# Optimization experiments

Hardware: AMD Instinct MI355X
Metric: run time of the kernel (lower is better)

The kernel has to match this reference:

```python
import jax, jax.numpy as jnp
import numpy as np

NEG_INF = -9e15
ALPHA = 0.2  # LeakyReLU negative slope

N = 4096
NFEAT = 512
NHID = 256
NEMBED = 128
NHEADS = 4
OUT1 = NHID // NHEADS   # 64
OUT2 = NEMBED // NHEADS # 32


def _gat_layer(x, adj_mask, W, a):
    # x: [N, F_in]; adj_mask: [N, N] bool; W: [H, F_in, F_out]; a: [H, 2*F_out]
    Fo = W.shape[-1]
    Wh = jnp.einsum('nf,hfo->hno', x, W)                     # [H, N, Fo]
    a_src = jnp.einsum('hno,ho->hn', Wh, a[:, :Fo])          # [H, N]
    a_dst = jnp.einsum('hno,ho->hn', Wh, a[:, Fo:])          # [H, N]
    e = a_src[:, :, None] + a_dst[:, None, :]                # [H, N, N]
    e = jax.nn.leaky_relu(e, negative_slope=ALPHA)
    e = jnp.where(adj_mask[None, :, :], e, NEG_INF)
    att = jax.nn.softmax(e, axis=-1)                         # [H, N, N]
    h = jnp.einsum('hnm,hmo->hno', att, Wh)                  # [H, N, Fo]
    h = jax.nn.elu(h)                                        # concat=True -> ELU
    # concat heads: [N, H*Fo]
    return jnp.transpose(h, (1, 0, 2)).reshape(x.shape[0], -1)


def setup_inputs() -> dict:
    key = jax.random.key(0)
    k1, k2, k3, k4, k5, k6 = jax.random.split(key, 6)
    x = jax.random.normal(k1, (N, NFEAT), dtype=jnp.float32)
    adj = (jax.random.uniform(k2, (N, N)) < 0.01).astype(jnp.float32)
    # per-head GAT params, xavier-uniform-like init (stacked over heads)
    def xavier(k, shape, fan):
        bound = np.sqrt(6.0 / fan)
        return jax.random.uniform(k, shape, minval=-bound, maxval=bound, dtype=jnp.float32)
    W1 = xavier(k3, (NHEADS, NFEAT, OUT1), NFEAT + OUT1)
    a1 = xavier(k4, (NHEADS, 2 * OUT1), 2 * OUT1 + 1)
    W2 = xavier(k5, (NHEADS, NHID, OUT2), NHID + OUT2)
    a2 = xavier(k6, (NHEADS, 2 * OUT2), 2 * OUT2 + 1)
    return {'x': x, 'adj': adj, 'W1': W1, 'a1': a1, 'W2': W2, 'a2': a2}


def reference(x, adj, W1, a1, W2, a2):
    # eval mode: dropout is identity
    adj_mask = adj > 0
    h1 = _gat_layer(x, adj_mask, W1, a1)    # [N, NHID]
    h2 = _gat_layer(h1, adj_mask, W2, a2)   # [N, NEMBED]
    return h2
```

## Files before the change

kernel.cpp:

```cpp
#include <hip/hip_runtime.h>
#include <hip/hip_bf16.h>
#include <cstdint>
#include <cstddef>

#define NNODES 4096
#define NHEADS 4
#define NBR_STRIDE 128

typedef __attribute__((ext_vector_type(8))) short bf16x8v;
typedef __attribute__((ext_vector_type(4))) float f32x4;

__device__ inline unsigned short bf16_rn(float f) {
    unsigned int u = __float_as_uint(f);
    u += 0x7FFFu + ((u >> 16) & 1u);
    return (unsigned short)(u >> 16);
}
__device__ inline float bf16_f32(unsigned short s) {
    return __uint_as_float(((unsigned int)s) << 16);
}

__global__ __launch_bounds__(256) void build_nbr_kernel(
    const float* __restrict__ adj, int* __restrict__ nbr, int* __restrict__ deg) {
    int wave = threadIdx.x >> 6;
    int lane = threadIdx.x & 63;
    int row = blockIdx.x * 4 + wave;
    const float4* arow = reinterpret_cast<const float4*>(adj + (size_t)row * NNODES);
    unsigned long long lt = (1ull << lane) - 1ull;
    int base = 0;
    #pragma unroll 4
    for (int it = 0; it < NNODES / 256; ++it) {
        float4 v = arow[it * 64 + lane];
        bool b0 = v.x > 0.f, b1 = v.y > 0.f, b2 = v.z > 0.f, b3 = v.w > 0.f;
        unsigned long long m0 = __ballot(b0);
        unsigned long long m1 = __ballot(b1);
        unsigned long long m2 = __ballot(b2);
        unsigned long long m3 = __ballot(b3);
        int pre = __popcll(m0 & lt) + __popcll(m1 & lt) +
                  __popcll(m2 & lt) + __popcll(m3 & lt);
        int pos = base + pre;
        int colb = it * 256 + lane * 4;
        if (b0) { if (pos < NBR_STRIDE) nbr[row * NBR_STRIDE + pos] = colb;     pos++; }
        if (b1) { if (pos < NBR_STRIDE) nbr[row * NBR_STRIDE + pos] = colb + 1; pos++; }
        if (b2) { if (pos < NBR_STRIDE) nbr[row * NBR_STRIDE + pos] = colb + 2; pos++; }
        if (b3) { if (pos < NBR_STRIDE) nbr[row * NBR_STRIDE + pos] = colb + 3; pos++; }
        base += __popcll(m0) + __popcll(m1) + __popcll(m2) + __popcll(m3);
    }
    if (lane == 0) deg[row] = base < NBR_STRIDE ? base : NBR_STRIDE;
}

__global__ __launch_bounds__(256) void pack_b_both_kernel(
    const float* __restrict__ W1, const float* __restrict__ W2,
    unsigned short* __restrict__ B1h, unsigned short* __restrict__ B1l,
    unsigned short* __restrict__ B2h, unsigned short* __restrict__ B2l) {
    int t = blockIdx.x * 256 + threadIdx.x;
    if (t < 256 * 512) {
        int n = t >> 9, k = t & 511;
        int h = n >> 6, o = n & 63;
        float v = W1[((size_t)h * 512 + k) * 64 + o];
        unsigned short hi = bf16_rn(v);
        B1h[t] = hi;
        B1l[t] = bf16_rn(v - bf16_f32(hi));
    } else {
        int u = t - 256 * 512;
        if (u < 128 * 256) {
            int n = u >> 8, k = u & 255;
            int h = n >> 5, o = n & 31;
            float v = W2[((size_t)h * 256 + k) * 32 + o];
            unsigned short hi = bf16_rn(v);
            B2h[u] = hi;
            B2l[u] = bf16_rn(v - bf16_f32(hi));
        }
    }
}

template <int K, int N>
__global__ __launch_bounds__(256) void gemm_split_kernel(
    const float* __restrict__ A,
    const unsigned short* __restrict__ Bh, const unsigned short* __restrict__ Bl,
    float* __restrict__ C) {
    constexpr int BM = 32, BN = 64, BK = 64, LP = BK + 8;
    __shared__ unsigned short Alh[BM][LP], All[BM][LP];
    __shared__ unsigned short Blh[BN][LP], Bll[BN][LP];
    int tid = threadIdx.x;
    int wave = tid >> 6, lane = tid & 63;
    int rowBase = blockIdx.x * BM;
    int colBase = blockIdx.y * BN;
    int wr = wave >> 1, wc = wave & 1;
    int lr = lane & 15, lk = lane >> 4;
    f32x4 acc0 = {0.f, 0.f, 0.f, 0.f};
    f32x4 acc1 = {0.f, 0.f, 0.f, 0.f};
    int ar = tid >> 3;
    int ac = (tid & 7) * 8;
    for (int k0 = 0; k0 < K; k0 += BK) {
        float4 a0 = *reinterpret_cast<const float4*>(&A[(size_t)(rowBase + ar) * K + k0 + ac]);
        float4 a1 = *reinterpret_cast<const float4*>(&A[(size_t)(rowBase + ar) * K + k0 + ac + 4]);
        uint4 bh0 = *reinterpret_cast<const uint4*>(&Bh[(size_t)(colBase + ar) * K + k0 + ac]);
        uint4 bl0 = *reinterpret_cast<const uint4*>(&Bl[(size_t)(colBase + ar) * K + k0 + ac]);
        uint4 bh1 = *reinterpret_cast<const uint4*>(&Bh[(size_t)(colBase + 32 + ar) * K + k0 + ac]);
        uint4 bl1 = *reinterpret_cast<const uint4*>(&Bl[(size_t)(colBase + 32 + ar) * K + k0 + ac]);
        __syncthreads();
        ushort4 h4, l4;
        h4.x = bf16_rn(a0.x); l4.x = bf16_rn(a0.x - bf16_f32(h4.x));
        h4.y = bf16_rn(a0.y); l4.y = bf16_rn(a0.y - bf16_f32(h4.y));
        h4.z = bf16_rn(a0.z); l4.z = bf16_rn(a0.z - bf16_f32(h4.z));
        h4.w = bf16_rn(a0.w); l4.w = bf16_rn(a0.w - bf16_f32(h4.w));
        *reinterpret_cast<ushort4*>(&Alh[ar][ac]) = h4;
        *reinterpret_cast<ushort4*>(&All[ar][ac]) = l4;
        h4.x = bf16_rn(a1.x); l4.x = bf16_rn(a1.x - bf16_f32(h4.x));
        h4.y = bf16_rn(a1.y); l4.y = bf16_rn(a1.y - bf16_f32(h4.y));
        h4.z = bf16_rn(a1.z); l4.z = bf16_rn(a1.z - bf16_f32(h4.z));
        h4.w = bf16_rn(a1.w); l4.w = bf16_rn(a1.w - bf16_f32(h4.w));
        *reinterpret_cast<ushort4*>(&Alh[ar][ac + 4]) = h4;
        *reinterpret_cast<ushort4*>(&All[ar][ac + 4]) = l4;
        *reinterpret_cast<uint4*>(&Blh[ar][ac]) = bh0;
        *reinterpret_cast<uint4*>(&Bll[ar][ac]) = bl0;
        *reinterpret_cast<uint4*>(&Blh[32 + ar][ac]) = bh1;
        *reinterpret_cast<uint4*>(&Bll[32 + ar][ac]) = bl1;
        __syncthreads();
        #pragma unroll
        for (int ks = 0; ks < 2; ++ks) {
            int kb = ks * 32 + lk * 8;
            bf16x8v ah = *reinterpret_cast<const bf16x8v*>(&Alh[wr * 16 + lr][kb]);
            bf16x8v al = *reinterpret_cast<const bf16x8v*>(&All[wr * 16 + lr][kb]);
            bf16x8v b0h = *reinterpret_cast<const bf16x8v*>(&Blh[wc * 32 + lr][kb]);
            bf16x8v b0l = *reinterpret_cast<const bf16x8v*>(&Bll[wc * 32 + lr][kb]);
            bf16x8v b1h = *reinterpret_cast<const bf16x8v*>(&Blh[wc * 32 + 16 + lr][kb]);
            bf16x8v b1l = *reinterpret_cast<const bf16x8v*>(&Bll[wc * 32 + 16 + lr][kb]);
            acc0 = __builtin_amdgcn_mfma_f32_16x16x32_bf16(ah, b0h, acc0, 0, 0, 0);
            acc0 = __builtin_amdgcn_mfma_f32_16x16x32_bf16(ah, b0l, acc0, 0, 0, 0);
            acc0 = __builtin_amdgcn_mfma_f32_16x16x32_bf16(al, b0h, acc0, 0, 0, 0);
            acc1 = __builtin_amdgcn_mfma_f32_16x16x32_bf16(ah, b1h, acc1, 0, 0, 0);
            acc1 = __builtin_amdgcn_mfma_f32_16x16x32_bf16(ah, b1l, acc1, 0, 0, 0);
            acc1 = __builtin_amdgcn_mfma_f32_16x16x32_bf16(al, b1h, acc1, 0, 0, 0);
        }
    }
    int crow = rowBase + wr * 16 + lk * 4;
    int ccol = colBase + wc * 32 + lr;
    #pragma unroll
    for (int r = 0; r < 4; ++r) {
        C[(size_t)(crow + r) * N + ccol]      = acc0[r];
        C[(size_t)(crow + r) * N + ccol + 16] = acc1[r];
    }
}

template <int FO>
__global__ __launch_bounds__(256) void adot_kernel(
    const float* __restrict__ Wh, const float* __restrict__ a,
    float* __restrict__ asrc, float* __restrict__ adst) {
    int t = blockIdx.x * blockDim.x + threadIdx.x;
    if (t >= NNODES * NHEADS) return;
    int n = t >> 2, h = t & 3;
    const float4* row = reinterpret_cast<const float4*>(Wh + (size_t)n * (NHEADS * FO) + h * FO);
    const float4* ah  = reinterpret_cast<const float4*>(a + h * 2 * FO);
    float s = 0.f, d = 0.f;
    #pragma unroll
    for (int o = 0; o < FO / 4; ++o) {
        float4 w = row[o];
        float4 u = ah[o];
        float4 v = ah[o + FO / 4];
        s += w.x * u.x + w.y * u.y + w.z * u.z + w.w * u.w;
        d += w.x * v.x + w.y * v.y + w.z * v.z + w.w * v.w;
    }
    asrc[h * NNODES + n] = s;
    adst[h * NNODES + n] = d;
}

template <int FO>
__global__ __launch_bounds__(256) void agg_kernel(
    const float* __restrict__ Wh,
    const float* __restrict__ asrc, const float* __restrict__ adst,
    const int* __restrict__ nbr, const int* __restrict__ deg,
    float* __restrict__ out) {
    __shared__ float2 sw[4][NBR_STRIDE];
    int wslot = threadIdx.x >> 6;
    int lane = threadIdx.x & 63;
    int wid = blockIdx.x * 4 + wslot;
    int n = wid >> 2, h = wid & 3;
    int dg = deg[n];
    const int* lst = nbr + n * NBR_STRIDE;
    float my_as = asrc[h * NNODES + n];

    int c0 = 0, c1 = 0;
    float e0 = -1e30f, e1 = -1e30f;
    if (lane < dg) {
        c0 = lst[lane];
        float e = my_as + adst[h * NNODES + c0];
        e0 = e >= 0.f ? e : 0.2f * e;
    }
    if (lane + 64 < dg) {
        c1 = lst[lane + 64];
        float e = my_as + adst[h * NNODES + c1];
        e1 = e >= 0.f ? e : 0.2f * e;
    }
    float m = fmaxf(e0, e1);
    #pragma unroll
    for (int s = 32; s; s >>= 1) m = fmaxf(m, __shfl_xor(m, s));
    float p0 = (lane < dg) ? __expf(e0 - m) : 0.f;
    float p1 = (lane + 64 < dg) ? __expf(e1 - m) : 0.f;
    float denom = p0 + p1;
    #pragma unroll
    for (int s = 32; s; s >>= 1) denom += __shfl_xor(denom, s);
    float inv = 1.0f / denom;

    if (lane < dg)      sw[wslot][lane]      = make_float2(p0 * inv, __int_as_float(c0));
    if (lane + 64 < dg) sw[wslot][lane + 64] = make_float2(p1 * inv, __int_as_float(c1));
    __syncthreads();

    constexpr int STRIDE = NHEADS * FO;
    constexpr int LPR = FO / 4;
    constexpr int NPS = 64 / LPR;
    int sub = lane / LPR;
    int dim4 = (lane % LPR) * 4;
    const float* whp = Wh + h * FO + dim4;
    f32x4 acc = {0.f, 0.f, 0.f, 0.f};
    int main_n = (dg / (4 * NPS)) * (4 * NPS);
    int k = 0;
    for (; k < main_n; k += 4 * NPS) {
        #pragma unroll
        for (int u = 0; u < 4; ++u) {
            float2 w = sw[wslot][k + u * NPS + sub];
            int col = __float_as_int(w.y);
            float4 v = *reinterpret_cast<const float4*>(&whp[(size_t)col * STRIDE]);
            acc[0] += w.x * v.x;
            acc[1] += w.x * v.y;
            acc[2] += w.x * v.z;
            acc[3] += w.x * v.w;
        }
    }
    for (; k < dg; k += NPS) {
        if (k + sub < dg) {
            float2 w = sw[wslot][k + sub];
            int col = __float_as_int(w.y);
            float4 v = *reinterpret_cast<const float4*>(&whp[(size_t)col * STRIDE]);
            acc[0] += w.x * v.x;
            acc[1] += w.x * v.y;
            acc[2] += w.x * v.z;
            acc[3] += w.x * v.w;
        }
    }
    #pragma unroll
    for (int s = LPR; s < 64; s <<= 1) {
        acc[0] += __shfl_xor(acc[0], s);
        acc[1] += __shfl_xor(acc[1], s);
        acc[2] += __shfl_xor(acc[2], s);
        acc[3] += __shfl_xor(acc[3], s);
    }
    if (lane < LPR) {
        float4 r;
        r.x = acc[0] > 0.f ? acc[0] : expm1f(acc[0]);
        r.y = acc[1] > 0.f ? acc[1] : expm1f(acc[1]);
        r.z = acc[2] > 0.f ? acc[2] : expm1f(acc[2]);
        r.w = acc[3] > 0.f ? acc[3] : expm1f(acc[3]);
        *reinterpret_cast<float4*>(&out[(size_t)n * STRIDE + h * FO + dim4]) = r;
    }
}

extern "C" void kernel_launch(void* const* d_in, const int* in_sizes, int n_in,
                              void* d_out, int out_size, void* d_ws, size_t ws_size,
                              hipStream_t stream) {
    const float* x   = (const float*)d_in[0];
    const float* adj = (const float*)d_in[1];
    const float* W1  = (const float*)d_in[2];
    const float* a1  = (const float*)d_in[3];
    const float* W2  = (const float*)d_in[4];
    const float* a2  = (const float*)d_in[5];
    float* out = (float*)d_out;

    char* p = (char*)d_ws;
    auto alloc = [&](size_t bytes) -> void* {
        void* r = (void*)p;
        p += (bytes + 255) & ~(size_t)255;
        return r;
    };
    int*   nbr = (int*)alloc((size_t)NNODES * NBR_STRIDE * 4);
    int*   deg = (int*)alloc((size_t)NNODES * 4);
    unsigned short* B1h = (unsigned short*)alloc((size_t)256 * 512 * 2);
    unsigned short* B1l = (unsigned short*)alloc((size_t)256 * 512 * 2);
    unsigned short* B2h = (unsigned short*)alloc((size_t)128 * 256 * 2);
    unsigned short* B2l = (unsigned short*)alloc((size_t)128 * 256 * 2);
    float* Wh1 = (float*)alloc((size_t)NNODES * 256 * 4);
    float* as1 = (float*)alloc((size_t)NHEADS * NNODES * 4);
    float* ad1 = (float*)alloc((size_t)NHEADS * NNODES * 4);
    float* h1  = (float*)alloc((size_t)NNODES * 256 * 4);
    float* Wh2 = (float*)alloc((size_t)NNODES * 128 * 4);
    float* as2 = (float*)alloc((size_t)NHEADS * NNODES * 4);
    float* ad2 = (float*)alloc((size_t)NHEADS * NNODES * 4);

    pack_b_both_kernel<<<dim3((256 * 512 + 128 * 256) / 256), dim3(256), 0, stream>>>(
        W1, W2, B1h, B1l, B2h, B2l);
    build_nbr_kernel<<<dim3(NNODES / 4), dim3(256), 0, stream>>>(adj, nbr, deg);

    gemm_split_kernel<512, 256><<<dim3(NNODES / 32, 256 / 64), dim3(256), 0, stream>>>(
        x, B1h, B1l, Wh1);
    adot_kernel<64><<<dim3(NNODES * NHEADS / 256), dim3(256), 0, stream>>>(
        Wh1, a1, as1, ad1);
    agg_kernel<64><<<dim3(NNODES * NHEADS / 4), dim3(256), 0, stream>>>(
        Wh1, as1, ad1, nbr, deg, h1);

    gemm_split_kernel<256, 128><<<dim3(NNODES / 32, 128 / 64), dim3(256), 0, stream>>>(
        h1, B2h, B2l, Wh2);
    adot_kernel<32><<<dim3(NNODES * NHEADS / 256), dim3(256), 0, stream>>>(
        Wh2, a2, as2, ad2);
    agg_kernel<32><<<dim3(NNODES * NHEADS / 4), dim3(256), 0, stream>>>(
        Wh2, as2, ad2, nbr, deg, out);
}
```

Measured before the change: 77.90 us.

## Fuse weight packing, attention dot products and neighbor build into GEMM kernels

Removes the separate weight pre-pack kernel: each GEMM block now loads fp32 W directly and splits it into bf16 hi/lo in shared memory. The a_src/a_dst dot products are computed in the GEMM epilogue with cross-lane shuffles and a small shared-memory reduction, which drops the adot kernels. Neighbor-list construction runs in the same launch as the first GEMM by partitioning blocks. Together this cuts the launch count from 8 to 4 and avoids re-reading Wh, at the cost of redundant weight conversion in every block and transposed, likely bank-conflicting LDS stores for B.

```diff
diff --git a/kernel.cpp b/kernel.cpp
--- a/kernel.cpp
+++ b/kernel.cpp
@@ -19,11 +19,12 @@
     return __uint_as_float(((unsigned int)s) << 16);
 }
 
-__global__ __launch_bounds__(256) void build_nbr_kernel(
-    const float* __restrict__ adj, int* __restrict__ nbr, int* __restrict__ deg) {
+__device__ inline void build_nbr_body(
+    const float* __restrict__ adj, int* __restrict__ nbr, int* __restrict__ deg,
+    int rowblk) {
     int wave = threadIdx.x >> 6;
     int lane = threadIdx.x & 63;
-    int row = blockIdx.x * 4 + wave;
+    int row = rowblk * 4 + wave;
     const float4* arow = reinterpret_cast<const float4*>(adj + (size_t)row * NNODES);
     unsigned long long lt = (1ull << lane) - 1ull;
     int base = 0;
@@ -48,43 +49,20 @@
     if (lane == 0) deg[row] = base < NBR_STRIDE ? base : NBR_STRIDE;
 }
 
-__global__ __launch_bounds__(256) void pack_b_both_kernel(
-    const float* __restrict__ W1, const float* __restrict__ W2,
-    unsigned short* __restrict__ B1h, unsigned short* __restrict__ B1l,
-    unsigned short* __restrict__ B2h, unsigned short* __restrict__ B2l) {
-    int t = blockIdx.x * 256 + threadIdx.x;
-    if (t < 256 * 512) {
-        int n = t >> 9, k = t & 511;
-        int h = n >> 6, o = n & 63;
-        float v = W1[((size_t)h * 512 + k) * 64 + o];
-        unsigned short hi = bf16_rn(v);
-        B1h[t] = hi;
-        B1l[t] = bf16_rn(v - bf16_f32(hi));
-    } else {
-        int u = t - 256 * 512;
-        if (u < 128 * 256) {
-            int n = u >> 8, k = u & 255;
-            int h = n >> 5, o = n & 31;
-            float v = W2[((size_t)h * 256 + k) * 32 + o];
-            unsigned short hi = bf16_rn(v);
-            B2h[u] = hi;
-            B2l[u] = bf16_rn(v - bf16_f32(hi));
-        }
-    }
-}
-
-template <int K, int N>
-__global__ __launch_bounds__(256) void gemm_split_kernel(
-    const float* __restrict__ A,
-    const unsigned short* __restrict__ Bh, const unsigned short* __restrict__ Bl,
-    float* __restrict__ C) {
+template <int K, int N, int FO>
+__device__ inline void gemm_body(
+    const float* __restrict__ A, const float* __restrict__ W,
+    const float* __restrict__ a, float* __restrict__ C,
+    float* __restrict__ asrc, float* __restrict__ adst,
+    int bx, int by) {
     constexpr int BM = 32, BN = 64, BK = 64, LP = BK + 8;
     __shared__ unsigned short Alh[BM][LP], All[BM][LP];
     __shared__ unsigned short Blh[BN][LP], Bll[BN][LP];
+    __shared__ float reds[2][BM], redd[2][BM];
     int tid = threadIdx.x;
     int wave = tid >> 6, lane = tid & 63;
-    int rowBase = blockIdx.x * BM;
-    int colBase = blockIdx.y * BN;
+    int rowBase = bx * BM;
+    int colBase = by * BN;
     int wr = wave >> 1, wc = wave & 1;
     int lr = lane & 15, lk = lane >> 4;
     f32x4 acc0 = {0.f, 0.f, 0.f, 0.f};
@@ -94,10 +72,19 @@
     for (int k0 = 0; k0 < K; k0 += BK) {
         float4 a0 = *reinterpret_cast<const float4*>(&A[(size_t)(rowBase + ar) * K + k0 + ac]);
         float4 a1 = *reinterpret_cast<const float4*>(&A[(size_t)(rowBase + ar) * K + k0 + ac + 4]);
-        uint4 bh0 = *reinterpret_cast<const uint4*>(&Bh[(size_t)(colBase + ar) * K + k0 + ac]);
-        uint4 bl0 = *reinterpret_cast<const uint4*>(&Bl[(size_t)(colBase + ar) * K + k0 + ac]);
-        uint4 bh1 = *reinterpret_cast<const uint4*>(&Bh[(size_t)(colBase + 32 + ar) * K + k0 + ac]);
-        uint4 bl1 = *reinterpret_cast<const uint4*>(&Bl[(size_t)(colBase + 32 + ar) * K + k0 + ac]);
+        float4 bw[4];
+        int bkr[4], bc4[4], bo[4], bh[4];
+        #pragma unroll
+        for (int i = 0; i < 4; ++i) {
+            int idx = tid + i * 256;
+            bkr[i] = idx >> 4;
+            bc4[i] = (idx & 15) * 4;
+            int n0 = colBase + bc4[i];
+            bh[i] = n0 / FO;
+            bo[i] = n0 % FO;
+            bw[i] = *reinterpret_cast<const float4*>(
+                &W[((size_t)bh[i] * K + k0 + bkr[i]) * FO + bo[i]]);
+        }
         __syncthreads();
         ushort4 h4, l4;
         h4.x = bf16_rn(a0.x); l4.x = bf16_rn(a0.x - bf16_f32(h4.x));
@@ -112,10 +99,19 @@
         h4.w = bf16_rn(a1.w); l4.w = bf16_rn(a1.w - bf16_f32(h4.w));
         *reinterpret_cast<ushort4*>(&Alh[ar][ac + 4]) = h4;
         *reinterpret_cast<ushort4*>(&All[ar][ac + 4]) = l4;
-        *reinterpret_cast<uint4*>(&Blh[ar][ac]) = bh0;
-        *reinterpret_cast<uint4*>(&Bll[ar][ac]) = bl0;
-        *reinterpret_cast<uint4*>(&Blh[32 + ar][ac]) = bh1;
-        *reinterpret_cast<uint4*>(&Bll[32 + ar][ac]) = bl1;
+        #pragma unroll
+        for (int i = 0; i < 4; ++i) {
+            float4 v = bw[i];
+            unsigned short hh, ll;
+            hh = bf16_rn(v.x); ll = bf16_rn(v.x - bf16_f32(hh));
+            Blh[bc4[i] + 0][bkr[i]] = hh; Bll[bc4[i] + 0][bkr[i]] = ll;
+            hh = bf16_rn(v.y); ll = bf16_rn(v.y - bf16_f32(hh));
+            Blh[bc4[i] + 1][bkr[i]] = hh; Bll[bc4[i] + 1][bkr[i]] = ll;
+            hh = bf16_rn(v.z); ll = bf16_rn(v.z - bf16_f32(hh));
+            Blh[bc4[i] + 2][bkr[i]] = hh; Bll[bc4[i] + 2][bkr[i]] = ll;
+            hh = bf16_rn(v.w); ll = bf16_rn(v.w - bf16_f32(hh));
+            Blh[bc4[i] + 3][bkr[i]] = hh; Bll[bc4[i] + 3][bkr[i]] = ll;
+        }
         __syncthreads();
         #pragma unroll
         for (int ks = 0; ks < 2; ++ks) {
@@ -141,28 +137,68 @@
         C[(size_t)(crow + r) * N + ccol]      = acc0[r];
         C[(size_t)(crow + r) * N + ccol + 16] = acc1[r];
     }
-}
-
-template <int FO>
-__global__ __launch_bounds__(256) void adot_kernel(
-    const float* __restrict__ Wh, const float* __restrict__ a,
-    float* __restrict__ asrc, float* __restrict__ adst) {
-    int t = blockIdx.x * blockDim.x + threadIdx.x;
-    if (t >= NNODES * NHEADS) return;
-    int n = t >> 2, h = t & 3;
-    const float4* row = reinterpret_cast<const float4*>(Wh + (size_t)n * (NHEADS * FO) + h * FO);
-    const float4* ah  = reinterpret_cast<const float4*>(a + h * 2 * FO);
-    float s = 0.f, d = 0.f;
-    #pragma unroll
-    for (int o = 0; o < FO / 4; ++o) {
-        float4 w = row[o];
-        float4 u = ah[o];
-        float4 v = ah[o + FO / 4];
-        s += w.x * u.x + w.y * u.y + w.z * u.z + w.w * u.w;
-        d += w.x * v.x + w.y * v.y + w.z * v.z + w.w * v.w;
-    }
-    asrc[h * NNODES + n] = s;
-    adst[h * NNODES + n] = d;
+    int n0 = colBase + wc * 32 + lr;
+    int hh = n0 / FO;
+    int o0 = n0 % FO;
+    int o1 = o0 + 16;
+    const float* av = a + hh * 2 * FO;
+    float aS0 = av[o0], aS1 = av[o1];
+    float aD0 = av[FO + o0], aD1 = av[FO + o1];
+    float sv[4], dv[4];
+    #pragma unroll
+    for (int r = 0; r < 4; ++r) {
+        sv[r] = acc0[r] * aS0 + acc1[r] * aS1;
+        dv[r] = acc0[r] * aD0 + acc1[r] * aD1;
+        #pragma unroll
+        for (int msk = 1; msk < 16; msk <<= 1) {
+            sv[r] += __shfl_xor(sv[r], msk);
+            dv[r] += __shfl_xor(dv[r], msk);
+        }
+    }
+    if constexpr (FO == 64) {
+        if (lr == 0) {
+            #pragma unroll
+            for (int r = 0; r < 4; ++r) {
+                reds[wc][wr * 16 + lk * 4 + r] = sv[r];
+                redd[wc][wr * 16 + lk * 4 + r] = dv[r];
+            }
+        }
+        __syncthreads();
+        if (tid < BM) {
+            int row = tid;
+            asrc[by * NNODES + rowBase + row] = reds[0][row] + reds[1][row];
+            adst[by * NNODES + rowBase + row] = redd[0][row] + redd[1][row];
+        }
+    } else {
+        if (lr == 0) {
+            #pragma unroll
+            for (int r = 0; r < 4; ++r) {
+                asrc[hh * NNODES + rowBase + wr * 16 + lk * 4 + r] = sv[r];
+                adst[hh * NNODES + rowBase + wr * 16 + lk * 4 + r] = dv[r];
+            }
+        }
+    }
+}
+
+__global__ __launch_bounds__(256) void fused1_kernel(
+    const float* __restrict__ adj, int* __restrict__ nbr, int* __restrict__ deg,
+    const float* __restrict__ x, const float* __restrict__ W1,
+    const float* __restrict__ a1, float* __restrict__ Wh1,
+    float* __restrict__ as1, float* __restrict__ ad1) {
+    int b = blockIdx.x;
+    if (b < NNODES / 4) {
+        build_nbr_body(adj, nbr, deg, b);
+    } else {
+        int g = b - NNODES / 4;
+        gemm_body<512, 256, 64>(x, W1, a1, Wh1, as1, ad1, g & 127, g >> 7);
+    }
+}
+
+__global__ __launch_bounds__(256) void gemm2_kernel(
+    const float* __restrict__ h1, const float* __restrict__ W2,
+    const float* __restrict__ a2, float* __restrict__ Wh2,
+    float* __restrict__ as2, float* __restrict__ ad2) {
+    gemm_body<256, 128, 32>(h1, W2, a2, Wh2, as2, ad2, blockIdx.x, blockIdx.y);
 }
 
 template <int FO>
@@ -274,10 +310,6 @@
     };
     int*   nbr = (int*)alloc((size_t)NNODES * NBR_STRIDE * 4);
     int*   deg = (int*)alloc((size_t)NNODES * 4);
-    unsigned short* B1h = (unsigned short*)alloc((size_t)256 * 512 * 2);
-    unsigned short* B1l = (unsigned short*)alloc((size_t)256 * 512 * 2);
-    unsigned short* B2h = (unsigned short*)alloc((size_t)128 * 256 * 2);
-    unsigned short* B2l = (unsigned short*)alloc((size_t)128 * 256 * 2);
     float* Wh1 = (float*)alloc((size_t)NNODES * 256 * 4);
     float* as1 = (float*)alloc((size_t)NHEADS * NNODES * 4);
     float* ad1 = (float*)alloc((size_t)NHEADS * NNODES * 4);
@@ -286,21 +318,13 @@
     float* as2 = (float*)alloc((size_t)NHEADS * NNODES * 4);
     float* ad2 = (float*)alloc((size_t)NHEADS * NNODES * 4);
 
-    pack_b_both_kernel<<<dim3((256 * 512 + 128 * 256) / 256), dim3(256), 0, stream>>>(
-        W1, W2, B1h, B1l, B2h, B2l);
-    build_nbr_kernel<<<dim3(NNODES / 4), dim3(256), 0, stream>>>(adj, nbr, deg);
-
-    gemm_split_kernel<512, 256><<<dim3(NNODES / 32, 256 / 64), dim3(256), 0, stream>>>(
-        x, B1h, B1l, Wh1);
-    adot_kernel<64><<<dim3(NNODES * NHEADS / 256), dim3(256), 0, stream>>>(
-        Wh1, a1, as1, ad1);
+    fused1_kernel<<<dim3(NNODES / 4 + 512), dim3(256), 0, stream>>>(
+        adj, nbr, deg, x, W1, a1, Wh1, as1, ad1);
     agg_kernel<64><<<dim3(NNODES * NHEADS / 4), dim3(256), 0, stream>>>(
         Wh1, as1, ad1, nbr, deg, h1);
 
-    gemm_split_kernel<256, 128><<<dim3(NNODES / 32, 128 / 64), dim3(256), 0, stream>>>(
-        h1, B2h, B2l, Wh2);
-    adot_kernel<32><<<dim3(NNODES * NHEADS / 256), dim3(256), 0, stream>>>(
-        Wh2, a2, as2, ad2);
+    gemm2_kernel<<<dim3(NNODES / 32, 2), dim3(256), 0, stream>>>(
+        h1, W2, a2, Wh2, as2, ad2);
     agg_kernel<32><<<dim3(NNODES * NHEADS / 4), dim3(256), 0, stream>>>(
         Wh2, as2, ad2, nbr, deg, out);
 }
```

Measured after the change: 85.38 us. 1.1x slower.
